# Kernel optimization log

Hardware: AMD Instinct MI355X
Metric: run time of the kernel (lower is better)

## Reference

```python
import jax, jax.numpy as jnp
import numpy as np

B = 16
NT, NH_, NW_, T_, H_, W_ = 4, 14, 14, 4, 1, 1
C = 768
NHEAD = 12
HD = C // NHEAD
SCALE = 1.0 / float(np.sqrt(HD))
TT = NT * T_            # 16 temporal slices
T2 = TT // 2            # 8 after even/odd split
HW = (NH_ * H_) * (NW_ * W_)  # 196 spatial tokens
TOKENS = NT * NH_ * NW_ * T_ * H_ * W_


def setup_inputs() -> dict:
    key = jax.random.key(0)
    ks = jax.random.split(key, 14)
    def lin(k, din, dout):
        return jax.random.normal(k, (din, dout), jnp.float32) * 0.02
    return {
        "x_in": jax.random.normal(ks[0], (B, TOKENS, C), jnp.float32),
        "Wq_d": lin(ks[1], C, C),      "bq_d": jnp.zeros((C,), jnp.float32),
        "Wkv_a": lin(ks[2], C, 2 * C), "bkv_a": jnp.zeros((2 * C,), jnp.float32),
        "Wq_a": lin(ks[3], C, C),      "bq_a": jnp.zeros((C,), jnp.float32),
        "Wkv_d": lin(ks[4], C, 2 * C), "bkv_d": jnp.zeros((2 * C,), jnp.float32),
        "Wp_d": lin(ks[5], C, C),      "bp_d": jnp.zeros((C,), jnp.float32),
        "Wp_a": lin(ks[6], C, C),      "bp_a": jnp.zeros((C,), jnp.float32),
    }


def _cross_attn(q_x, kv_x, Wq, bq, Wkv, bkv):
    # q_x, kv_x: (b, t, hw, c)
    b, t, hw, c = q_x.shape
    q = (q_x @ Wq + bq).reshape(b, t, hw, NHEAD, HD)
    kv = (kv_x @ Wkv + bkv).reshape(b, t, hw, 2, NHEAD, HD)
    k, v = kv[..., 0, :, :], kv[..., 1, :, :]
    s = jnp.einsum('btqhd,btkhd->bthqk', q, k) * SCALE
    p = jax.nn.softmax(s, axis=-1)
    o = jnp.einsum('bthqk,btkhd->btqhd', p, v)
    return o.reshape(b, t, hw, c)


def reference(x_in, Wq_d, bq_d, Wkv_a, bkv_a, Wq_a, bq_a, Wkv_d, bkv_d,
              Wp_d, bp_d, Wp_a, bp_a):
    b = x_in.shape[0]
    # einops: b (nt nh nw t h w) c -> b (nt t) (nh h) (nw w) c
    x = x_in.reshape(b, NT, NH_, NW_, T_, H_, W_, C)
    x = x.transpose(0, 1, 4, 2, 5, 3, 6, 7).reshape(b, TT, NH_ * H_, NW_ * W_, C)
    x_skip = x                                   # (b, TT, h, w, c)
    x = x.reshape(b, TT, HW, C)                  # (b, TT, hw, c)
    x_a = x[:, 0::2]                             # (b, T2, hw, c) approx
    x_d = x[:, 1::2]                             # (b, T2, hw, c) detail

    # detail cross-attends to approx, subtract-update
    _d = _cross_attn(x_d, x_a, Wq_d, bq_d, Wkv_a, bkv_a)
    _d = jax.nn.gelu(_d @ Wp_d + bp_d, approximate=False)
    x_d = x_d - _d
    # approx cross-attends to updated detail, add-update
    _a = _cross_attn(x_a, x_d, Wq_a, bq_a, Wkv_d, bkv_d)
    _a = jax.nn.gelu(_a @ Wp_a + bp_a, approximate=False)
    x_a = x_a + _a

    # relaxed_constrain: pooled-skip minus channel-mean of x_a
    xs = x_skip.reshape(b, TT, HW, C)
    pooled = xs.reshape(b, T2, 2, HW, C).mean(axis=2)   # avg_pool2d (2,1)
    pool_a = pooled.mean(axis=-1) - x_a.mean(axis=-1)   # (b, T2, hw)

    # SSL=False: mean over channels, keepdim (torch layout b,1,t,hw)
    x_d_out = x_d.mean(axis=-1)[:, None, :, :]          # (b, 1, T2, hw)
    return (pool_a, x_d_out)
```

## Files before the change

kernel.cpp:

```cpp
#include <hip/hip_runtime.h>

typedef __bf16 bf16;
typedef __attribute__((ext_vector_type(8))) __bf16 bf16x8;
typedef __attribute__((ext_vector_type(4))) __bf16 bf16x4;
typedef __attribute__((ext_vector_type(2))) __bf16 bf16x2;
typedef __attribute__((ext_vector_type(4))) float f32x4;
typedef __attribute__((ext_vector_type(4))) unsigned int u32x4;

#define TOKENS 3136
#define CC 768
#define KVC 1536
#define S196 196
#define M_ROWS 25088
#define BATCH 16

__device__ __forceinline__ float bf2f(bf16 x) { return (float)x; }
__device__ __forceinline__ bf16 f2bf(float x) { return (bf16)x; }

__device__ __forceinline__ float gelu_exact(float x) {
    return 0.5f * x * (1.0f + erff(x * 0.70710678118654752f));
}

__device__ __forceinline__ unsigned int packbf(float a, float b) {
    bf16x2 v; v[0] = (bf16)a; v[1] = (bf16)b;
    return __builtin_bit_cast(unsigned int, v);
}

#define GLOAD_LDS16(gp, lp) \
    __builtin_amdgcn_global_load_lds((const __attribute__((address_space(1))) void*)(gp), \
                                     (__attribute__((address_space(3))) void*)(lp), 16, 0, 0)

__global__ __launch_bounds__(256)
void transpose_w(const float* __restrict__ W, bf16* __restrict__ Wt, int K, int N)
{
    __shared__ float tle[32][33];
    int k0 = blockIdx.x * 32, n0 = blockIdx.y * 32;
    int tx = threadIdx.x & 31, ty = threadIdx.x >> 5;
    for (int r = ty; r < 32; r += 8)
        tle[r][tx] = W[(long)(k0 + r) * N + n0 + tx];
    __syncthreads();
    for (int r = ty; r < 32; r += 8)
        Wt[(long)(n0 + r) * K + k0 + tx] = f2bf(tle[tx][r]);
}

__global__ __launch_bounds__(256)
void conv_bias(const float* b0, const float* b1, const float* b2,
               const float* b3, const float* b4, const float* b5,
               bf16* __restrict__ dst)
{
    const float* srcs[6] = {b0, b1, b2, b3, b4, b5};
    const int sizes[6]   = {768, 1536, 768, 1536, 768, 768};
    const int offs[6]    = {0, 768, 2304, 3072, 4608, 5376};
    int which = blockIdx.x;
    const float* s = srcs[which];
    int n = sizes[which];
    bf16* d = dst + offs[which];
    for (int i = threadIdx.x; i < n; i += 256)
        d[i] = f2bf(s[i]);
}

__global__ __launch_bounds__(256)
void reorder_split(const float* __restrict__ x_in, bf16* __restrict__ xa,
                   bf16* __restrict__ xd)
{
    long idx = (long)blockIdx.x * 256 + threadIdx.x;
    const long total = (long)BATCH * 16 * S196 * 96;
    if (idx >= total) return;
    int  c8  = (int)(idx % 96) * 8;
    long row = idx / 96;
    int  s   = (int)(row % S196);
    long r2  = row / S196;
    int  tt  = (int)(r2 & 15);
    int  b   = (int)(r2 >> 4);
    int  nt  = tt >> 2, t = tt & 3;
    int  nh  = s / 14,  nw = s % 14;
    long src  = ((long)b * TOKENS + ((nt * 14 + nh) * 14 + nw) * 4 + t) * CC + c8;
    bf16* dst = (tt & 1) ? xd : xa;
    long doff = ((long)(b * 8 + (tt >> 1)) * S196 + s) * CC + c8;
    const float* sp = x_in + src;
    f32x4 a = *(const f32x4*)sp;
    f32x4 c = *(const f32x4*)(sp + 4);
    bf16x8 v;
    v[0] = f2bf(a[0]); v[1] = f2bf(a[1]); v[2] = f2bf(a[2]); v[3] = f2bf(a[3]);
    v[4] = f2bf(c[0]); v[5] = f2bf(c[1]); v[6] = f2bf(c[2]); v[7] = f2bf(c[3]);
    *(bf16x8*)(dst + doff) = v;
}

template<int EPI>
__global__ __launch_bounds__(256)
void gemm_bt(const bf16* __restrict__ A, const bf16* __restrict__ Bt,
             const bf16* __restrict__ bias, const bf16* __restrict__ res,
             bf16* __restrict__ C, int N, int K)
{
    constexpr int BM = 128, BN = 128, BK = 32;
    __shared__ alignas(16) bf16 sA[BM * BK];
    __shared__ alignas(16) bf16 sB[BN * BK];
    const int tid  = threadIdx.x;
    const int lane = tid & 63, wave = tid >> 6;
    const int wm   = wave >> 1, wn = wave & 1;
    const int quad = lane >> 4, l16 = lane & 15;
    const long m0 = (long)blockIdx.x * BM;
    const long n0 = (long)blockIdx.y * BN;

    f32x4 acc[4][4] = {};

    for (int kt = 0; kt < K; kt += BK) {
        if (kt) __syncthreads();
        #pragma unroll
        for (int c = 0; c < 2; ++c) {
            int ci = (wave * 2 + c) * 64 + lane;
            int r  = ci >> 2, kc = ci & 3;
            const bf16* ga = A  + (m0 + r) * K + kt + kc * 8;
            const bf16* gb = Bt + (n0 + r) * K + kt + kc * 8;
            bf16* la = sA + (wave * 2 + c) * 512;
            bf16* lb = sB + (wave * 2 + c) * 512;
            GLOAD_LDS16(ga, la);
            GLOAD_LDS16(gb, lb);
        }
        __syncthreads();

        bf16x8 af[4], bfr[4];
        #pragma unroll
        for (int mi = 0; mi < 4; ++mi)
            af[mi] = *(const bf16x8*)(sA + (wm * 64 + mi * 16 + l16) * BK + quad * 8);
        #pragma unroll
        for (int ni = 0; ni < 4; ++ni)
            bfr[ni] = *(const bf16x8*)(sB + (wn * 64 + ni * 16 + l16) * BK + quad * 8);
        #pragma unroll
        for (int mi = 0; mi < 4; ++mi)
            #pragma unroll
            for (int ni = 0; ni < 4; ++ni)
                acc[mi][ni] = __builtin_amdgcn_mfma_f32_16x16x32_bf16(af[mi], bfr[ni], acc[mi][ni], 0, 0, 0);
    }

    #pragma unroll
    for (int mi = 0; mi < 4; ++mi) {
        #pragma unroll
        for (int ni = 0; ni < 4; ++ni) {
            int mg = (int)m0 + wm * 64 + mi * 16 + quad * 4;
            int ng = (int)n0 + wn * 64 + ni * 16 + l16;
            float bn = bf2f(bias[ng]);
            #pragma unroll
            for (int r = 0; r < 4; ++r) {
                float x = acc[mi][ni][r] + bn;
                long off = (long)(mg + r) * N + ng;
                if (EPI == 0)      C[off] = f2bf(x);
                else if (EPI == 1) C[off] = f2bf(bf2f(res[off]) - gelu_exact(x));
                else               C[off] = f2bf(bf2f(res[off]) + gelu_exact(x));
            }
        }
    }
}

#define KSTR 72
#define VSTR 264

__global__ __launch_bounds__(256)
void attn_mfma(const bf16* __restrict__ Q, const bf16* __restrict__ KV,
               bf16* __restrict__ O)
{
    const int h  = blockIdx.x;
    const int bj = blockIdx.y;
    __shared__ alignas(16) bf16 Ks[208 * KSTR];
    __shared__ alignas(16) bf16 Vt[64 * VSTR];
    const int tid = threadIdx.x, lane = tid & 63, wave = tid >> 6;
    const int quad = lane >> 4, l16 = lane & 15;

    const bf16* qg = Q  + (long)bj * S196 * CC  + h * 64;
    const bf16* kg = KV + (long)bj * S196 * KVC + h * 64;
    const bf16* vg = kg + CC;

    for (int i = tid; i < 208 * 8; i += 256) {
        int r = i >> 3, c8 = (i & 7) * 8;
        bf16x8 v = {};
        if (r < S196) v = *(const bf16x8*)(kg + (long)r * KVC + c8);
        *(bf16x8*)(Ks + r * KSTR + c8) = v;
    }
    for (int i = tid; i < 256 * 8; i += 256) {
        int g   = i >> 6;
        int c8  = (g & 7) * 8;
        int tok = (g >> 3) * 64 + (i & 63);
        bf16x8 v = {};
        if (tok < S196) v = *(const bf16x8*)(vg + (long)tok * KVC + c8);
        #pragma unroll
        for (int j = 0; j < 8; ++j)
            Vt[(c8 + j) * VSTR + tok] = v[j];
    }
    __syncthreads();

    for (int qt = wave; qt < 13; qt += 4) {
        int qrow = qt * 16 + l16; if (qrow > 195) qrow = 195;
        const bf16* qrp = qg + (long)qrow * CC + quad * 8;
        bf16x8 qf0 = *(const bf16x8*)(qrp);
        bf16x8 qf1 = *(const bf16x8*)(qrp + 32);

        f32x4 st[13];
        #pragma unroll
        for (int rt = 0; rt < 13; ++rt) st[rt] = (f32x4){0.f, 0.f, 0.f, 0.f};
        #pragma unroll
        for (int rt = 0; rt < 13; ++rt) {
            const bf16* kb = Ks + (rt * 16 + l16) * KSTR + quad * 8;
            bf16x8 kf0 = *(const bf16x8*)(kb);
            bf16x8 kf1 = *(const bf16x8*)(kb + 32);
            st[rt] = __builtin_amdgcn_mfma_f32_16x16x32_bf16(kf0, qf0, st[rt], 0, 0, 0);
            st[rt] = __builtin_amdgcn_mfma_f32_16x16x32_bf16(kf1, qf1, st[rt], 0, 0, 0);
        }

        const float SC = 0.125f;
        #pragma unroll
        for (int rt = 0; rt < 13; ++rt) {
            st[rt][0] *= SC; st[rt][1] *= SC; st[rt][2] *= SC; st[rt][3] *= SC;
        }
        if (quad != 0)
            st[12] = (f32x4){-1e30f, -1e30f, -1e30f, -1e30f};

        float m = -1e30f;
        #pragma unroll
        for (int rt = 0; rt < 13; ++rt)
            m = fmaxf(m, fmaxf(fmaxf(st[rt][0], st[rt][1]), fmaxf(st[rt][2], st[rt][3])));
        m = fmaxf(m, __shfl_xor(m, 16, 64));
        m = fmaxf(m, __shfl_xor(m, 32, 64));
        float sum = 0.f;
        #pragma unroll
        for (int rt = 0; rt < 13; ++rt) {
            st[rt][0] = __expf(st[rt][0] - m);
            st[rt][1] = __expf(st[rt][1] - m);
            st[rt][2] = __expf(st[rt][2] - m);
            st[rt][3] = __expf(st[rt][3] - m);
            sum += st[rt][0] + st[rt][1] + st[rt][2] + st[rt][3];
        }
        sum += __shfl_xor(sum, 16, 64);
        sum += __shfl_xor(sum, 32, 64);
        float inv = 1.0f / sum;

        unsigned int pk[13][2];
        #pragma unroll
        for (int rt = 0; rt < 13; ++rt) {
            pk[rt][0] = packbf(st[rt][0] * inv, st[rt][1] * inv);
            pk[rt][1] = packbf(st[rt][2] * inv, st[rt][3] * inv);
        }

        f32x4 ot[4];
        #pragma unroll
        for (int dt = 0; dt < 4; ++dt) ot[dt] = (f32x4){0.f, 0.f, 0.f, 0.f};
        #pragma unroll
        for (int c = 0; c < 7; ++c) {
            u32x4 fp;
            #pragma unroll
            for (int jp = 0; jp < 4; ++jp) {
                int jh = jp >> 1, rp = jp & 1;
                int srcb = ((((quad & 1) << 1) + jh) << 6) | (l16 << 2);
                int a = __builtin_amdgcn_ds_bpermute(srcb, (int)pk[2 * c][rp]);
                int b = (c < 6) ? __builtin_amdgcn_ds_bpermute(srcb, (int)pk[2 * c + 1][rp]) : 0;
                fp[jp] = (quad >> 1) ? (unsigned int)b : (unsigned int)a;
            }
            bf16x8 pB = __builtin_bit_cast(bf16x8, fp);
            #pragma unroll
            for (int dt = 0; dt < 4; ++dt) {
                bf16x8 vf = *(const bf16x8*)(Vt + (dt * 16 + l16) * VSTR + c * 32 + quad * 8);
                ot[dt] = __builtin_amdgcn_mfma_f32_16x16x32_bf16(vf, pB, ot[dt], 0, 0, 0);
            }
        }

        int token = qt * 16 + l16;
        if (token < S196) {
            bf16* op = O + ((long)bj * S196 + token) * CC + h * 64 + quad * 4;
            #pragma unroll
            for (int dt = 0; dt < 4; ++dt) {
                bf16x4 v;
                v[0] = f2bf(ot[dt][0]); v[1] = f2bf(ot[dt][1]);
                v[2] = f2bf(ot[dt][2]); v[3] = f2bf(ot[dt][3]);
                *(bf16x4*)(op + dt * 16) = v;
            }
        }
    }
}

__global__ __launch_bounds__(256)
void out_reduce(const float* __restrict__ x_in, const bf16* __restrict__ xa,
                const bf16* __restrict__ xd, float* __restrict__ out)
{
    int id = blockIdx.x;
    int s  = id % S196;
    int bj = id / S196;
    int j  = bj & 7, b = bj >> 3;
    int tid = threadIdx.x, lane = tid & 63, wave = tid >> 6;
    int nh = s / 14, nw = s % 14;

    float sum = 0.f;
    if (wave < 2) {
        int tt = 2 * j + wave;
        int nt = tt >> 2, t = tt & 3;
        const float* p = x_in + ((long)b * TOKENS + ((nt * 14 + nh) * 14 + nw) * 4 + t) * CC;
        for (int c = lane; c < CC; c += 64) sum += p[c];
    } else {
        const bf16* p = (wave == 2 ? xa : xd) + (long)id * CC;
        for (int c = lane; c < CC; c += 64) sum += bf2f(p[c]);
    }
    #pragma unroll
    for (int off = 32; off; off >>= 1) sum += __shfl_xor(sum, off, 64);

    __shared__ float r4[4];
    if (lane == 0) r4[wave] = sum;
    __syncthreads();
    if (tid == 0) {
        const float invC = 1.0f / 768.0f;
        out[id]          = (r4[0] + r4[1]) * 0.5f * invC - r4[2] * invC;
        out[M_ROWS + id] = r4[3] * invC;
    }
}

extern "C" void kernel_launch(void* const* d_in, const int* in_sizes, int n_in,
                              void* d_out, int out_size, void* d_ws, size_t ws_size,
                              hipStream_t stream)
{
    const float* x_in  = (const float*)d_in[0];
    const float* Wq_d  = (const float*)d_in[1];
    const float* bq_d  = (const float*)d_in[2];
    const float* Wkv_a = (const float*)d_in[3];
    const float* bkv_a = (const float*)d_in[4];
    const float* Wq_a  = (const float*)d_in[5];
    const float* bq_a  = (const float*)d_in[6];
    const float* Wkv_d = (const float*)d_in[7];
    const float* bkv_d = (const float*)d_in[8];
    const float* Wp_d  = (const float*)d_in[9];
    const float* bp_d  = (const float*)d_in[10];
    const float* Wp_a  = (const float*)d_in[11];
    const float* bp_a  = (const float*)d_in[12];
    float* out = (float*)d_out;

    char* w = (char*)d_ws;
    auto alloc = [&](size_t elems) {
        bf16* p = (bf16*)w;
        w += ((elems * 2 + 255) / 256) * 256;
        return p;
    };
    bf16* biasAll = alloc(6144);
    bf16* WtQd = alloc((size_t)768 * 768);
    bf16* WtKa = alloc((size_t)1536 * 768);
    bf16* WtQa = alloc((size_t)768 * 768);
    bf16* WtKd = alloc((size_t)1536 * 768);
    bf16* WtPd = alloc((size_t)768 * 768);
    bf16* WtPa = alloc((size_t)768 * 768);
    bf16* xa   = alloc((size_t)M_ROWS * 768);
    bf16* xd   = alloc((size_t)M_ROWS * 768);
    bf16* Qb   = alloc((size_t)M_ROWS * 768);
    bf16* KVb  = alloc((size_t)M_ROWS * 1536);
    bf16* Ob   = alloc((size_t)M_ROWS * 768);

    dim3 blk(256);
    transpose_w<<<dim3(24, 24), blk, 0, stream>>>(Wq_d,  WtQd, 768, 768);
    transpose_w<<<dim3(24, 48), blk, 0, stream>>>(Wkv_a, WtKa, 768, 1536);
    transpose_w<<<dim3(24, 24), blk, 0, stream>>>(Wq_a,  WtQa, 768, 768);
    transpose_w<<<dim3(24, 48), blk, 0, stream>>>(Wkv_d, WtKd, 768, 1536);
    transpose_w<<<dim3(24, 24), blk, 0, stream>>>(Wp_d,  WtPd, 768, 768);
    transpose_w<<<dim3(24, 24), blk, 0, stream>>>(Wp_a,  WtPa, 768, 768);
    conv_bias<<<dim3(6), blk, 0, stream>>>(bq_d, bkv_a, bq_a, bkv_d, bp_d, bp_a, biasAll);

    long total_chunks = (long)BATCH * 16 * S196 * 96;
    int  rblocks = (int)((total_chunks + 255) / 256);
    reorder_split<<<rblocks, blk, 0, stream>>>(x_in, xa, xd);

    const bf16* Bq_d  = biasAll;
    const bf16* Bkv_a = biasAll + 768;
    const bf16* Bq_a  = biasAll + 2304;
    const bf16* Bkv_d = biasAll + 3072;
    const bf16* Bp_d  = biasAll + 4608;
    const bf16* Bp_a  = biasAll + 5376;

    dim3 g768(196, 6), g1536(196, 12);

    gemm_bt<0><<<g768,  blk, 0, stream>>>(xd, WtQd, Bq_d,  nullptr, Qb,  768,  768);
    gemm_bt<0><<<g1536, blk, 0, stream>>>(xa, WtKa, Bkv_a, nullptr, KVb, 1536, 768);
    attn_mfma<<<dim3(12, 128), blk, 0, stream>>>(Qb, KVb, Ob);
    gemm_bt<1><<<g768,  blk, 0, stream>>>(Ob, WtPd, Bp_d,  xd,      xd,  768,  768);

    gemm_bt<0><<<g768,  blk, 0, stream>>>(xa, WtQa, Bq_a,  nullptr, Qb,  768,  768);
    gemm_bt<0><<<g1536, blk, 0, stream>>>(xd, WtKd, Bkv_d, nullptr, KVb, 1536, 768);
    attn_mfma<<<dim3(12, 128), blk, 0, stream>>>(Qb, KVb, Ob);
    gemm_bt<2><<<g768,  blk, 0, stream>>>(Ob, WtPa, Bp_a,  xa,      xa,  768,  768);

    out_reduce<<<M_ROWS, blk, 0, stream>>>(x_in, xa, xd, out);
}
```

Measured before the change: 984.4 us.

## Fuse xa Q/KV projections into one GEMM, group-swizzle tiles, split final reduction

Concatenates the Wkv_a and Wq_a weights so a single GEMM over xa produces K, V and the second-stage Q, replacing two passes over xa with one. The GEMM grid becomes 1D with grouped-M tile swizzling for better L2 reuse of A rows. The final reduction no longer reads fp32 x_in: the pooled term is computed early from bf16 xa/xd with a wave-per-row kernel, and the end kernel also uses wave-per-row. The cost is an extra reduction kernel, plus skip-mean precision that now comes from bf16 copies rather than fp32 input.

```diff
diff --git a/kernel.cpp b/kernel.cpp
--- a/kernel.cpp
+++ b/kernel.cpp
@@ -9,7 +9,6 @@
 
 #define TOKENS 3136
 #define CC 768
-#define KVC 1536
 #define S196 196
 #define M_ROWS 25088
 #define BATCH 16
@@ -86,21 +85,73 @@
     *(bf16x8*)(dst + doff) = v;
 }
 
+__device__ __forceinline__ float row_sum768(const bf16* __restrict__ p, int lane)
+{
+    float s = 0.f;
+    bf16x8 v = *(const bf16x8*)(p + lane * 8);
+    #pragma unroll
+    for (int j = 0; j < 8; ++j) s += bf2f(v[j]);
+    if (lane < 32) {
+        bf16x8 w = *(const bf16x8*)(p + 512 + lane * 8);
+        #pragma unroll
+        for (int j = 0; j < 8; ++j) s += bf2f(w[j]);
+    }
+    #pragma unroll
+    for (int off = 32; off; off >>= 1) s += __shfl_xor(s, off, 64);
+    return s;
+}
+
+__global__ __launch_bounds__(256)
+void pool_ad(const bf16* __restrict__ xa, const bf16* __restrict__ xd,
+             float* __restrict__ pool0)
+{
+    int id = blockIdx.x * 4 + (threadIdx.x >> 6);
+    int lane = threadIdx.x & 63;
+    float sa = row_sum768(xa + (long)id * CC, lane);
+    float sd = row_sum768(xd + (long)id * CC, lane);
+    if (lane == 0) pool0[id] = (sa + sd) * (0.5f / 768.0f);
+}
+
+__global__ __launch_bounds__(256)
+void out_final(const bf16* __restrict__ xa, const bf16* __restrict__ xd,
+               const float* __restrict__ pool0, float* __restrict__ out)
+{
+    int id = blockIdx.x * 4 + (threadIdx.x >> 6);
+    int lane = threadIdx.x & 63;
+    float sa = row_sum768(xa + (long)id * CC, lane);
+    float sd = row_sum768(xd + (long)id * CC, lane);
+    if (lane == 0) {
+        out[id]          = pool0[id] - sa * (1.0f / 768.0f);
+        out[M_ROWS + id] = sd * (1.0f / 768.0f);
+    }
+}
+
 template<int EPI>
 __global__ __launch_bounds__(256)
 void gemm_bt(const bf16* __restrict__ A, const bf16* __restrict__ Bt,
              const bf16* __restrict__ bias, const bf16* __restrict__ res,
-             bf16* __restrict__ C, int N, int K)
-{
-    constexpr int BM = 128, BN = 128, BK = 32;
+             bf16* __restrict__ C, int ldc, int K, int mTiles, int nTiles)
+{
+    constexpr int BM = 128, BK = 32;
     __shared__ alignas(16) bf16 sA[BM * BK];
-    __shared__ alignas(16) bf16 sB[BN * BK];
+    __shared__ alignas(16) bf16 sB[BM * BK];
     const int tid  = threadIdx.x;
     const int lane = tid & 63, wave = tid >> 6;
     const int wm   = wave >> 1, wn = wave & 1;
     const int quad = lane >> 4, l16 = lane & 15;
-    const long m0 = (long)blockIdx.x * BM;
-    const long n0 = (long)blockIdx.y * BN;
+
+    const int GM = 16;
+    int pid   = blockIdx.x;
+    int group = GM * nTiles;
+    int gid   = pid / group;
+    int rem   = pid - gid * group;
+    int first = gid * GM;
+    int gm    = (mTiles - first < GM) ? (mTiles - first) : GM;
+    int bm    = first + rem % gm;
+    int bn    = rem / gm;
+
+    const long m0 = (long)bm * BM;
+    const long n0 = (long)bn * BM;
 
     f32x4 acc[4][4] = {};
 
@@ -139,11 +190,11 @@
         for (int ni = 0; ni < 4; ++ni) {
             int mg = (int)m0 + wm * 64 + mi * 16 + quad * 4;
             int ng = (int)n0 + wn * 64 + ni * 16 + l16;
-            float bn = bf2f(bias[ng]);
+            float bn_ = bf2f(bias[ng]);
             #pragma unroll
             for (int r = 0; r < 4; ++r) {
-                float x = acc[mi][ni][r] + bn;
-                long off = (long)(mg + r) * N + ng;
+                float x = acc[mi][ni][r] + bn_;
+                long off = (long)(mg + r) * ldc + ng;
                 if (EPI == 0)      C[off] = f2bf(x);
                 else if (EPI == 1) C[off] = f2bf(bf2f(res[off]) - gelu_exact(x));
                 else               C[off] = f2bf(bf2f(res[off]) + gelu_exact(x));
@@ -156,7 +207,8 @@
 #define VSTR 264
 
 __global__ __launch_bounds__(256)
-void attn_mfma(const bf16* __restrict__ Q, const bf16* __restrict__ KV,
+void attn_mfma(const bf16* __restrict__ Q, int ldq,
+               const bf16* __restrict__ KV, int ldkv,
                bf16* __restrict__ O)
 {
     const int h  = blockIdx.x;
@@ -166,14 +218,14 @@
     const int tid = threadIdx.x, lane = tid & 63, wave = tid >> 6;
     const int quad = lane >> 4, l16 = lane & 15;
 
-    const bf16* qg = Q  + (long)bj * S196 * CC  + h * 64;
-    const bf16* kg = KV + (long)bj * S196 * KVC + h * 64;
+    const bf16* qg = Q  + (long)bj * S196 * ldq  + h * 64;
+    const bf16* kg = KV + (long)bj * S196 * ldkv + h * 64;
     const bf16* vg = kg + CC;
 
     for (int i = tid; i < 208 * 8; i += 256) {
         int r = i >> 3, c8 = (i & 7) * 8;
         bf16x8 v = {};
-        if (r < S196) v = *(const bf16x8*)(kg + (long)r * KVC + c8);
+        if (r < S196) v = *(const bf16x8*)(kg + (long)r * ldkv + c8);
         *(bf16x8*)(Ks + r * KSTR + c8) = v;
     }
     for (int i = tid; i < 256 * 8; i += 256) {
@@ -181,7 +233,7 @@
         int c8  = (g & 7) * 8;
         int tok = (g >> 3) * 64 + (i & 63);
         bf16x8 v = {};
-        if (tok < S196) v = *(const bf16x8*)(vg + (long)tok * KVC + c8);
+        if (tok < S196) v = *(const bf16x8*)(vg + (long)tok * ldkv + c8);
         #pragma unroll
         for (int j = 0; j < 8; ++j)
             Vt[(c8 + j) * VSTR + tok] = v[j];
@@ -190,7 +242,7 @@
 
     for (int qt = wave; qt < 13; qt += 4) {
         int qrow = qt * 16 + l16; if (qrow > 195) qrow = 195;
-        const bf16* qrp = qg + (long)qrow * CC + quad * 8;
+        const bf16* qrp = qg + (long)qrow * ldq + quad * 8;
         bf16x8 qf0 = *(const bf16x8*)(qrp);
         bf16x8 qf1 = *(const bf16x8*)(qrp + 32);
 
@@ -273,40 +325,6 @@
                 *(bf16x4*)(op + dt * 16) = v;
             }
         }
-    }
-}
-
-__global__ __launch_bounds__(256)
-void out_reduce(const float* __restrict__ x_in, const bf16* __restrict__ xa,
-                const bf16* __restrict__ xd, float* __restrict__ out)
-{
-    int id = blockIdx.x;
-    int s  = id % S196;
-    int bj = id / S196;
-    int j  = bj & 7, b = bj >> 3;
-    int tid = threadIdx.x, lane = tid & 63, wave = tid >> 6;
-    int nh = s / 14, nw = s % 14;
-
-    float sum = 0.f;
-    if (wave < 2) {
-        int tt = 2 * j + wave;
-        int nt = tt >> 2, t = tt & 3;
-        const float* p = x_in + ((long)b * TOKENS + ((nt * 14 + nh) * 14 + nw) * 4 + t) * CC;
-        for (int c = lane; c < CC; c += 64) sum += p[c];
-    } else {
-        const bf16* p = (wave == 2 ? xa : xd) + (long)id * CC;
-        for (int c = lane; c < CC; c += 64) sum += bf2f(p[c]);
-    }
-    #pragma unroll
-    for (int off = 32; off; off >>= 1) sum += __shfl_xor(sum, off, 64);
-
-    __shared__ float r4[4];
-    if (lane == 0) r4[wave] = sum;
-    __syncthreads();
-    if (tid == 0) {
-        const float invC = 1.0f / 768.0f;
-        out[id]          = (r4[0] + r4[1]) * 0.5f * invC - r4[2] * invC;
-        out[M_ROWS + id] = r4[3] * invC;
     }
 }
 
@@ -336,22 +354,22 @@
         return p;
     };
     bf16* biasAll = alloc(6144);
-    bf16* WtQd = alloc((size_t)768 * 768);
-    bf16* WtKa = alloc((size_t)1536 * 768);
-    bf16* WtQa = alloc((size_t)768 * 768);
-    bf16* WtKd = alloc((size_t)1536 * 768);
-    bf16* WtPd = alloc((size_t)768 * 768);
-    bf16* WtPa = alloc((size_t)768 * 768);
-    bf16* xa   = alloc((size_t)M_ROWS * 768);
-    bf16* xd   = alloc((size_t)M_ROWS * 768);
-    bf16* Qb   = alloc((size_t)M_ROWS * 768);
-    bf16* KVb  = alloc((size_t)M_ROWS * 1536);
-    bf16* Ob   = alloc((size_t)M_ROWS * 768);
+    bf16* WtQd  = alloc((size_t)768 * 768);
+    bf16* WtACat= alloc((size_t)2304 * 768);
+    bf16* WtKd  = alloc((size_t)1536 * 768);
+    bf16* WtPd  = alloc((size_t)768 * 768);
+    bf16* WtPa  = alloc((size_t)768 * 768);
+    bf16* xa    = alloc((size_t)M_ROWS * 768);
+    bf16* xd    = alloc((size_t)M_ROWS * 768);
+    bf16* Qb    = alloc((size_t)M_ROWS * 768);
+    bf16* QKVa  = alloc((size_t)M_ROWS * 2304);
+    bf16* Ob    = alloc((size_t)M_ROWS * 768);
+    float* pool0 = (float*)w; w += ((size_t)M_ROWS * 4 + 255) / 256 * 256;
 
     dim3 blk(256);
     transpose_w<<<dim3(24, 24), blk, 0, stream>>>(Wq_d,  WtQd, 768, 768);
-    transpose_w<<<dim3(24, 48), blk, 0, stream>>>(Wkv_a, WtKa, 768, 1536);
-    transpose_w<<<dim3(24, 24), blk, 0, stream>>>(Wq_a,  WtQa, 768, 768);
+    transpose_w<<<dim3(24, 48), blk, 0, stream>>>(Wkv_a, WtACat, 768, 1536);
+    transpose_w<<<dim3(24, 24), blk, 0, stream>>>(Wq_a,  WtACat + (size_t)1536 * 768, 768, 768);
     transpose_w<<<dim3(24, 48), blk, 0, stream>>>(Wkv_d, WtKd, 768, 1536);
     transpose_w<<<dim3(24, 24), blk, 0, stream>>>(Wp_d,  WtPd, 768, 768);
     transpose_w<<<dim3(24, 24), blk, 0, stream>>>(Wp_a,  WtPa, 768, 768);
@@ -360,25 +378,22 @@
     long total_chunks = (long)BATCH * 16 * S196 * 96;
     int  rblocks = (int)((total_chunks + 255) / 256);
     reorder_split<<<rblocks, blk, 0, stream>>>(x_in, xa, xd);
-
-    const bf16* Bq_d  = biasAll;
-    const bf16* Bkv_a = biasAll + 768;
-    const bf16* Bq_a  = biasAll + 2304;
-    const bf16* Bkv_d = biasAll + 3072;
-    const bf16* Bp_d  = biasAll + 4608;
-    const bf16* Bp_a  = biasAll + 5376;
-
-    dim3 g768(196, 6), g1536(196, 12);
-
-    gemm_bt<0><<<g768,  blk, 0, stream>>>(xd, WtQd, Bq_d,  nullptr, Qb,  768,  768);
-    gemm_bt<0><<<g1536, blk, 0, stream>>>(xa, WtKa, Bkv_a, nullptr, KVb, 1536, 768);
-    attn_mfma<<<dim3(12, 128), blk, 0, stream>>>(Qb, KVb, Ob);
-    gemm_bt<1><<<g768,  blk, 0, stream>>>(Ob, WtPd, Bp_d,  xd,      xd,  768,  768);
-
-    gemm_bt<0><<<g768,  blk, 0, stream>>>(xa, WtQa, Bq_a,  nullptr, Qb,  768,  768);
-    gemm_bt<0><<<g1536, blk, 0, stream>>>(xd, WtKd, Bkv_d, nullptr, KVb, 1536, 768);
-    attn_mfma<<<dim3(12, 128), blk, 0, stream>>>(Qb, KVb, Ob);
-    gemm_bt<2><<<g768,  blk, 0, stream>>>(Ob, WtPa, Bp_a,  xa,      xa,  768,  768);
-
-    out_reduce<<<M_ROWS, blk, 0, stream>>>(x_in, xa, xd, out);
-}
+    pool_ad<<<M_ROWS / 4, blk, 0, stream>>>(xa, xd, pool0);
+
+    const bf16* Bq_d   = biasAll;
+    const bf16* Bkva_qa= biasAll + 768;
+    const bf16* Bkv_d  = biasAll + 3072;
+    const bf16* Bp_d   = biasAll + 4608;
+    const bf16* Bp_a   = biasAll + 5376;
+
+    gemm_bt<0><<<196 * 6,  blk, 0, stream>>>(xd, WtQd,  Bq_d,    nullptr, Qb,   768,  768, 196, 6);
+    gemm_bt<0><<<196 * 18, blk, 0, stream>>>(xa, WtACat, Bkva_qa, nullptr, QKVa, 2304, 768, 196, 18);
+    attn_mfma<<<dim3(12, 128), blk, 0, stream>>>(Qb, 768, QKVa, 2304, Ob);
+    gemm_bt<1><<<196 * 6,  blk, 0, stream>>>(Ob, WtPd, Bp_d, xd, xd, 768, 768, 196, 6);
+
+    gemm_bt<0><<<196 * 12, blk, 0, stream>>>(xd, WtKd, Bkv_d, nullptr, QKVa, 2304, 768, 196, 12);
+    attn_mfma<<<dim3(12, 128), blk, 0, stream>>>(QKVa + 1536, 2304, QKVa, 2304, Ob);
+    gemm_bt<2><<<196 * 6,  blk, 0, stream>>>(Ob, WtPa, Bp_a, xa, xa, 768, 768, 196, 6);
+
+    out_final<<<M_ROWS / 4, blk, 0, stream>>>(xa, xd, pool0, out);
+}
```

Result: faster. 869.1 us (-11.7%).
